# Kernel optimization log

Measured on AMD Instinct MI355X. Metric: run time of the kernel, lower is better.

The kernel has to match this reference:

```python
import jax, jax.numpy as jnp
import numpy as np

B, S, D, H, HD, L, V = 32, 512, 512, 8, 64, 6, 64000
EPS = 1e-5

def _layer_norm(x, g, b):
    mu = jnp.mean(x, axis=-1, keepdims=True)
    var = jnp.mean(jnp.square(x - mu), axis=-1, keepdims=True)
    return (x - mu) * jax.lax.rsqrt(var + EPS) * g + b

def _sinusoidal_pe():
    pos = np.arange(S)[:, None].astype(np.float32)
    div = np.exp(np.arange(0, D, 2).astype(np.float32) * -(np.log(10000.0) / D))
    pe = np.zeros((S, D), dtype=np.float32)
    pe[:, 0::2] = np.sin(pos * div)
    pe[:, 1::2] = np.cos(pos * div)
    return jnp.asarray(pe)

def setup_inputs() -> dict:
    key = jax.random.key(0)
    ks = jax.random.split(key, 8)
    std = 0.02
    return {
        'tokens': jax.random.randint(ks[0], (B, S), 0, V),
        'mask': jnp.ones((B, S), dtype=jnp.int32),
        'emb': jax.random.normal(ks[1], (V, D), jnp.float32) * std,
        'pe': _sinusoidal_pe(),
        'Wq': jax.random.normal(ks[2], (L, H, D, HD), jnp.float32) * std,
        'Wk': jax.random.normal(ks[3], (L, H, D, HD), jnp.float32) * std,
        'Wv': jax.random.normal(ks[4], (L, H, D, HD), jnp.float32) * std,
        'Wo': jax.random.normal(ks[5], (L, D, D), jnp.float32) * std,
        'ln1_g': jnp.ones((L, D), jnp.float32),
        'ln1_b': jnp.zeros((L, D), jnp.float32),
        'W1': jax.random.normal(ks[6], (L, D, 4 * D), jnp.float32) * std,
        'b1': jnp.zeros((L, 4 * D), jnp.float32),
        'W2': jax.random.normal(ks[7], (L, 4 * D, D), jnp.float32) * std,
        'b2': jnp.zeros((L, D), jnp.float32),
        'ln2_g': jnp.ones((L, D), jnp.float32),
        'ln2_b': jnp.zeros((L, D), jnp.float32),
    }

def reference(tokens, mask, emb, pe, Wq, Wk, Wv, Wo, ln1_g, ln1_b, W1, b1, W2, b2, ln2_g, ln2_b):
    # Eval mode: all dropouts are identity.
    x = emb[tokens] + pe[None, :S, :]               # [B,S,D]
    neg_inf = jnp.finfo(x.dtype).min
    mask_b = (mask == 0)[:, None, None, :]          # [B,1,1,S] broadcast over heads & queries
    scale = HD ** -0.5
    for l in range(L):
        q = jnp.einsum('bsd,hde->bhse', x, Wq[l])
        k = jnp.einsum('bsd,hde->bhse', x, Wk[l])
        v = jnp.einsum('bsd,hde->bhse', x, Wv[l])
        w = jnp.einsum('bhse,bhte->bhst', q, k) * scale
        w = jnp.where(mask_b, neg_inf, w)
        a = jax.nn.softmax(w, axis=-1)
        o = jnp.einsum('bhst,bhte->bhse', a, v)     # [B,H,S,HD]
        o = o.transpose(0, 2, 1, 3).reshape(x.shape[0], S, D)  # concat heads
        x = _layer_norm(x + o @ Wo[l], ln1_g[l], ln1_b[l])
        h = jax.nn.gelu(x @ W1[l] + b1[l], approximate=False) @ W2[l] + b2[l]
        x = _layer_norm(x + h, ln2_g[l], ln2_b[l])
    return x
```

## Files before the change

### kernel.cpp

```cpp
#include <hip/hip_runtime.h>

#define BB 32
#define SS 512
#define DD 512
#define HH 8
#define HDH 64
#define LL 6
#define DFF 2048
#define MM (BB*SS)

typedef __attribute__((ext_vector_type(4))) float f32x4;
typedef __attribute__((ext_vector_type(8))) short s16x8;
typedef __attribute__((ext_vector_type(4))) short s16x4;

__device__ __forceinline__ unsigned short f2bf(float f) {
    union { float f; unsigned u; } v; v.f = f;
    unsigned r = v.u + 0x7fffu + ((v.u >> 16) & 1u);
    return (unsigned short)(r >> 16);
}
__device__ __forceinline__ float bf2f(unsigned short b) {
    union { unsigned u; float f; } v; v.u = ((unsigned)b) << 16;
    return v.f;
}

__device__ __forceinline__ f32x4 mfma_bf16(s16x8 a, s16x8 b, f32x4 c) {
    asm("v_mfma_f32_16x16x32_bf16 %0, %1, %2, %0" : "+v"(c) : "v"(a), "v"(b));
    return c;
}

__device__ __forceinline__ void gload_lds16(const void* g, void* l) {
    __builtin_amdgcn_global_load_lds(
        (__attribute__((address_space(1))) void*)g,
        (__attribute__((address_space(3))) void*)l, 16, 0, 0);
}

__device__ __forceinline__ void tile_transpose_conv(
    const float* __restrict__ src, int srcPitch,
    unsigned short* __restrict__ dst, int dstPitch,
    float* lt)
{
    const int t = threadIdx.x;
    #pragma unroll
    for (int it = 0; it < 4; ++it) {
        int r = it * 16 + (t >> 4);
        int c = (t & 15) * 4;
        f32x4 v = *(const f32x4*)(src + (size_t)r * srcPitch + c);
        lt[r * 65 + c + 0] = v[0];
        lt[r * 65 + c + 1] = v[1];
        lt[r * 65 + c + 2] = v[2];
        lt[r * 65 + c + 3] = v[3];
    }
    __syncthreads();
    int nn = t >> 2;
    int kc = (t & 3) * 16;
    s16x8 o0, o1;
    #pragma unroll
    for (int i = 0; i < 8; ++i)  o0[i] = (short)f2bf(lt[(kc + i) * 65 + nn]);
    #pragma unroll
    for (int i = 0; i < 8; ++i)  o1[i] = (short)f2bf(lt[(kc + 8 + i) * 65 + nn]);
    *(s16x8*)(dst + (size_t)nn * dstPitch + kc) = o0;
    *(s16x8*)(dst + (size_t)nn * dstPitch + kc + 8) = o1;
}

__global__ __launch_bounds__(256) void k_tconv_qkv(const float* __restrict__ Wq,
                                                   const float* __restrict__ Wk,
                                                   const float* __restrict__ Wv,
                                                   unsigned short* __restrict__ dst) {
    __shared__ float lt[64 * 65];
    int bid = blockIdx.x;
    int which = bid / 384;
    int rem = bid - which * 384;
    int l = rem >> 6;
    int h = (rem >> 3) & 7;
    int kt = rem & 7;
    const float* W = which == 0 ? Wq : (which == 1 ? Wk : Wv);
    const float* srcT = W + (((size_t)(l * HH + h) * 512) + kt * 64) * 64;
    unsigned short* dstT = dst + ((size_t)l * 1536 + which * 512 + h * 64) * 512 + kt * 64;
    tile_transpose_conv(srcT, 64, dstT, 512, lt);
}

__global__ __launch_bounds__(256) void k_tconv_w(const float* __restrict__ src,
                                                 unsigned short* __restrict__ dst,
                                                 int K, int N) {
    __shared__ float lt[64 * 65];
    int tpb = (K >> 6) * (N >> 6);
    int bid = blockIdx.x;
    int l = bid / tpb;
    int rem = bid - l * tpb;
    int kt = rem / (N >> 6);
    int ntile = rem - kt * (N >> 6);
    const float* srcT = src + (size_t)l * K * N + (size_t)(kt * 64) * N + ntile * 64;
    unsigned short* dstT = dst + (size_t)l * N * K + (size_t)(ntile * 64) * K + kt * 64;
    tile_transpose_conv(srcT, N, dstT, K, lt);
}

__global__ __launch_bounds__(256) void k_embed(const int* __restrict__ tokens,
                                               const float* __restrict__ emb,
                                               const float* __restrict__ pe,
                                               float* __restrict__ x,
                                               unsigned short* __restrict__ xh) {
    int i = blockIdx.x * 256 + threadIdx.x;
    int row = i >> 7;
    int d4 = (i & 127) * 4;
    int srow = row & (SS - 1);
    int tok = tokens[row];
    f32x4 ev = *(const f32x4*)(emb + (size_t)tok*DD + d4);
    f32x4 pv = *(const f32x4*)(pe + (size_t)srow*DD + d4);
    f32x4 vv; s16x4 hv;
    #pragma unroll
    for (int j = 0; j < 4; ++j) {
        vv[j] = ev[j] + pv[j];
        hv[j] = (short)f2bf(vv[j]);
    }
    *(f32x4*)(x + (size_t)row*DD + d4) = vv;
    *(s16x4*)(xh + (size_t)row*DD + d4) = hv;
}

__global__ __launch_bounds__(128) void k_ln(const float* __restrict__ x,
                                            const unsigned short* __restrict__ y,
                                            const float* __restrict__ gg,
                                            const float* __restrict__ bb,
                                            float* __restrict__ xo,
                                            unsigned short* __restrict__ xh) {
    const int row = blockIdx.x;
    const int tid = threadIdx.x;
    __shared__ float red[4];
    f32x4 xv = *(const f32x4*)(x + (size_t)row*DD + tid*4);
    s16x4 yv = *(const s16x4*)(y + (size_t)row*DD + tid*4);
    f32x4 vv;
    #pragma unroll
    for (int j = 0; j < 4; ++j) vv[j] = xv[j] + bf2f((unsigned short)yv[j]);
    float sum = vv[0] + vv[1] + vv[2] + vv[3];
    #pragma unroll
    for (int off = 1; off < 64; off <<= 1) sum += __shfl_xor(sum, off);
    if ((tid & 63) == 0) red[tid >> 6] = sum;
    __syncthreads();
    float mu = (red[0] + red[1]) * (1.0f / 512.0f);
    float s2 = 0.0f;
    #pragma unroll
    for (int j = 0; j < 4; ++j) { float d = vv[j] - mu; s2 += d * d; }
    #pragma unroll
    for (int off = 1; off < 64; off <<= 1) s2 += __shfl_xor(s2, off);
    if ((tid & 63) == 0) red[2 + (tid >> 6)] = s2;
    __syncthreads();
    float var = (red[2] + red[3]) * (1.0f / 512.0f);
    float rs = rsqrtf(var + 1e-5f);
    f32x4 gv = *(const f32x4*)(gg + tid*4);
    f32x4 bv = *(const f32x4*)(bb + tid*4);
    f32x4 ov; s16x4 hv;
    #pragma unroll
    for (int j = 0; j < 4; ++j) {
        float o = (vv[j] - mu) * rs * gv[j] + bv[j];
        ov[j] = o;
        hv[j] = (short)f2bf(o);
    }
    *(f32x4*)(xo + (size_t)row*DD + tid*4) = ov;
    *(s16x4*)(xh + (size_t)row*DD + tid*4) = hv;
}

template<int EPI>
__global__ __launch_bounds__(256, 2) void k_gemm(
    const unsigned short* __restrict__ A, const unsigned short* __restrict__ Bt,
    unsigned short* __restrict__ ob,
    const float* __restrict__ bias, int N, int K, int nt)
{
    __shared__ short lds[2][2][4096];
    const int tid = threadIdx.x;
    const int lane = tid & 63;
    const int wid = tid >> 6;
    const int g = lane >> 4;
    const int t16 = lane & 15;

    int nwg = gridDim.x;
    int bid = blockIdx.x;
    int cpx = nwg >> 3;
    int swz = (bid & 7) * cpx + (bid >> 3);
    int bm = swz / nt;
    int bn = swz - bm * nt;

    const unsigned short* Ag = A  + (size_t)bm * 128 * K;
    const unsigned short* Bg = Bt + (size_t)bn * 128 * K;

    auto stage = [&](int buf, int k0) {
        #pragma unroll
        for (int i = 0; i < 2; ++i) {
            int slot = i * 256 + tid;
            int r = slot >> 2;
            int j = slot & 3;
            int js = j ^ ((r >> 1) & 3);
            size_t go = (size_t)r * K + k0 + js * 8;
            int lo = i * 2048 + wid * 512;
            gload_lds16(Ag + go, &lds[buf][0][lo]);
            gload_lds16(Bg + go, &lds[buf][1][lo]);
        }
    };

    f32x4 acc[4][4];
    #pragma unroll
    for (int a_ = 0; a_ < 4; ++a_)
        #pragma unroll
        for (int b_ = 0; b_ < 4; ++b_) acc[a_][b_] = (f32x4){0.f, 0.f, 0.f, 0.f};

    const int wm = wid >> 1, wn = wid & 1;
    stage(0, 0);
    __syncthreads();
    int nk = K >> 5;
    int buf = 0;
    for (int kt = 0; kt < nk; ++kt) {
        if (kt + 1 < nk) stage(buf ^ 1, (kt + 1) << 5);
        s16x8 af[4], bf_[4];
        #pragma unroll
        for (int mt = 0; mt < 4; ++mt) {
            int r = wm * 64 + mt * 16 + t16;
            af[mt] = *(const s16x8*)&lds[buf][0][r * 32 + ((g ^ ((r >> 1) & 3)) << 3)];
        }
        #pragma unroll
        for (int nt_ = 0; nt_ < 4; ++nt_) {
            int r = wn * 64 + nt_ * 16 + t16;
            bf_[nt_] = *(const s16x8*)&lds[buf][1][r * 32 + ((g ^ ((r >> 1) & 3)) << 3)];
        }
        #pragma unroll
        for (int mt = 0; mt < 4; ++mt)
            #pragma unroll
            for (int nt_ = 0; nt_ < 4; ++nt_)
                acc[mt][nt_] = mfma_bf16(af[mt], bf_[nt_], acc[mt][nt_]);
        __syncthreads();
        buf ^= 1;
    }

    #pragma unroll
    for (int mt = 0; mt < 4; ++mt)
        #pragma unroll
        for (int nt_ = 0; nt_ < 4; ++nt_) {
            int row0 = bm * 128 + wm * 64 + mt * 16 + g * 4;
            int col  = bn * 128 + wn * 64 + nt_ * 16 + t16;
            f32x4 v = acc[mt][nt_];
            float bv = (EPI == 2) ? bias[col] : 0.0f;
            #pragma unroll
            for (int r_ = 0; r_ < 4; ++r_) {
                size_t idx = (size_t)(row0 + r_) * N + col;
                if (EPI == 0) {
                    ob[idx] = f2bf(v[r_]);
                } else {
                    float tv = v[r_] + bv;
                    float ge = 0.5f * tv * (1.0f + erff(tv * 0.70710678118f));
                    ob[idx] = f2bf(ge);
                }
            }
        }
}

__global__ __launch_bounds__(512, 2) void k_gemm8(
    const unsigned short* __restrict__ A, const unsigned short* __restrict__ Bt,
    unsigned short* __restrict__ ob,
    const float* __restrict__ bias, int N, int K, int nt)
{
    extern __shared__ short lds[];
    const int tid = threadIdx.x;
    const int lane = tid & 63;
    const int wid = tid >> 6;
    const int g = lane >> 4;
    const int t16 = lane & 15;
    const int wm = wid >> 2, wn = wid & 3;

    int nwg = gridDim.x;
    int bid = blockIdx.x;
    int cpx = nwg >> 3;
    int swz = (bid & 7) * cpx + (bid >> 3);
    int bm = swz / nt;
    int bn = swz - bm * nt;

    const unsigned short* Ag = A  + (size_t)bm * 256 * K;
    const unsigned short* Bg = Bt + (size_t)bn * 128 * K;

    auto stage_unit = [&](int slot, int t, int unit) {
        const int k0 = t << 6;
        const unsigned short* src = (unit == 2) ? Bg : (Ag + (unit ? (size_t)128 * K : 0));
        short* dst0 = lds + slot * 24576 + (unit == 2 ? 16384 : unit * 8192);
        #pragma unroll
        for (int rr = 0; rr < 2; ++rr) {
            int rb = rr * 64 + wid * 8;
            int r_in = rb + (lane >> 3);
            int c = (lane & 7) ^ (r_in & 7);
            gload_lds16(src + (size_t)r_in * K + k0 + c * 8, dst0 + rb * 64);
        }
    };

    f32x4 acc[8][2];
    #pragma unroll
    for (int a_ = 0; a_ < 8; ++a_)
        #pragma unroll
        for (int b_ = 0; b_ < 2; ++b_) acc[a_][b_] = (f32x4){0.f, 0.f, 0.f, 0.f};

    const int nk = K >> 6;
    stage_unit(0, 0, 0); stage_unit(0, 0, 1); stage_unit(0, 0, 2);
    stage_unit(1, 1, 0); stage_unit(1, 1, 1); stage_unit(1, 1, 2);

    int slot = 0;
    for (int t = 0; t < nk; ++t) {
        if (t + 1 < nk) asm volatile("s_waitcnt vmcnt(6)" ::: "memory");
        else            asm volatile("s_waitcnt vmcnt(0)" ::: "memory");
        __builtin_amdgcn_s_barrier();
        __builtin_amdgcn_sched_barrier(0);

        int s2 = slot + 2; if (s2 >= 3) s2 -= 3;
        const short* As = lds + slot * 24576;
        const short* Bs = As + 16384;

        if (t + 2 < nk) { stage_unit(s2, t + 2, 0); stage_unit(s2, t + 2, 1); }
        s16x8 bfr[2][2];
        #pragma unroll
        for (int nn = 0; nn < 2; ++nn) {
            int row = wn * 32 + nn * 16 + t16;
            #pragma unroll
            for (int kk = 0; kk < 2; ++kk)
                bfr[nn][kk] = *(const s16x8*)&Bs[row * 64 + (((kk * 4 + g) ^ (row & 7)) << 3)];
        }
        {
            s16x8 afr[4][2];
            #pragma unroll
            for (int mm = 0; mm < 4; ++mm) {
                int row = wm * 128 + mm * 16 + t16;
                #pragma unroll
                for (int kk = 0; kk < 2; ++kk)
                    afr[mm][kk] = *(const s16x8*)&As[row * 64 + (((kk * 4 + g) ^ (row & 7)) << 3)];
            }
            __builtin_amdgcn_sched_barrier(0);
            __builtin_amdgcn_s_setprio(1);
            #pragma unroll
            for (int mm = 0; mm < 4; ++mm)
                #pragma unroll
                for (int nn = 0; nn < 2; ++nn)
                    #pragma unroll
                    for (int kk = 0; kk < 2; ++kk)
                        acc[mm][nn] = mfma_bf16(afr[mm][kk], bfr[nn][kk], acc[mm][nn]);
            __builtin_amdgcn_s_setprio(0);
            __builtin_amdgcn_sched_barrier(0);
        }
        if (t + 2 < nk) stage_unit(s2, t + 2, 2);
        {
            s16x8 afr[4][2];
            #pragma unroll
            for (int mm = 0; mm < 4; ++mm) {
                int row = wm * 128 + (mm + 4) * 16 + t16;
                #pragma unroll
                for (int kk = 0; kk < 2; ++kk)
                    afr[mm][kk] = *(const s16x8*)&As[row * 64 + (((kk * 4 + g) ^ (row & 7)) << 3)];
            }
            __builtin_amdgcn_sched_barrier(0);
            __builtin_amdgcn_s_setprio(1);
            #pragma unroll
            for (int mm = 0; mm < 4; ++mm)
                #pragma unroll
                for (int nn = 0; nn < 2; ++nn)
                    #pragma unroll
                    for (int kk = 0; kk < 2; ++kk)
                        acc[mm + 4][nn] = mfma_bf16(afr[mm][kk], bfr[nn][kk], acc[mm + 4][nn]);
            __builtin_amdgcn_s_setprio(0);
            __builtin_amdgcn_sched_barrier(0);
        }
        slot = slot + 1 == 3 ? 0 : slot + 1;
    }

    #pragma unroll
    for (int mm = 0; mm < 8; ++mm)
        #pragma unroll
        for (int nn = 0; nn < 2; ++nn) {
            int row0 = bm * 256 + wm * 128 + mm * 16 + g * 4;
            int col  = bn * 128 + wn * 32 + nn * 16 + t16;
            f32x4 v = acc[mm][nn];
            float bv = bias[col];
            #pragma unroll
            for (int r_ = 0; r_ < 4; ++r_)
                ob[(size_t)(row0 + r_) * N + col] = f2bf(v[r_] + bv);
        }
}

__global__ __launch_bounds__(1024, 4) void k_attn(
    const unsigned short* __restrict__ qkv, const int* __restrict__ mask,
    unsigned short* __restrict__ o)
{
    extern __shared__ short smem[];
    short* Kl = smem;
    short* Vl = smem + 32768;
    const int tid = threadIdx.x;
    const int lane = tid & 63, wid = tid >> 6;
    short* Pl = smem + 65536 + wid * 1024;
    const int b = blockIdx.x >> 3, h = blockIdx.x & 7;
    const unsigned short* base = qkv + (size_t)b * SS * 1536;
    const int qc = h * 64, kc = 512 + h * 64, vc = 1024 + h * 64;

    for (int c = tid; c < 4096; c += 1024) {
        int t = c >> 3, j = c & 7;
        s16x8 kv = *(const s16x8*)(base + (size_t)t * 1536 + kc + j * 8);
        *(s16x8*)(Kl + t * 64 + ((j ^ (t & 7)) << 3)) = kv;
    }
    {
        int unit = tid >> 1, half = tid & 1;
        int t0 = (unit >> 3) << 3, e0 = (unit & 7) << 3;
        s16x8 r0 = *(const s16x8*)(base + (size_t)(t0 + half*4 + 0) * 1536 + vc + e0);
        s16x8 r1 = *(const s16x8*)(base + (size_t)(t0 + half*4 + 1) * 1536 + vc + e0);
        s16x8 r2 = *(const s16x8*)(base + (size_t)(t0 + half*4 + 2) * 1536 + vc + e0);
        s16x8 r3 = *(const s16x8*)(base + (size_t)(t0 + half*4 + 3) * 1536 + vc + e0);
        #pragma unroll
        for (int j = 0; j < 8; ++j) {
            int e = e0 + j;
            int slot = (t0 >> 3) ^ (e & 7) ^ ((e >> 3) & 7);
            s16x4 w = (s16x4){r0[j], r1[j], r2[j], r3[j]};
            *(s16x4*)(Vl + e * 512 + (slot << 3) + (half << 2)) = w;
        }
    }
    const int g = lane >> 4, t16 = lane & 15;
    unsigned mbits = 0;
    for (int n2 = 0; n2 < 32; ++n2)
        if (mask[b * SS + n2 * 16 + t16] != 0) mbits |= (1u << n2);
    __syncthreads();

    for (int qi = 0; qi < 2; ++qi) {
        const int q0 = (wid * 2 + qi) * 16;
        s16x8 aq[2];
        #pragma unroll
        for (int ks = 0; ks < 2; ++ks)
            aq[ks] = *(const s16x8*)(base + (size_t)(q0 + t16) * 1536 + qc + ks * 32 + g * 8);

        f32x4 oacc[4];
        #pragma unroll
        for (int eo = 0; eo < 4; ++eo) oacc[eo] = (f32x4){0.f, 0.f, 0.f, 0.f};
        float mx[4] = {-3.0e38f, -3.0e38f, -3.0e38f, -3.0e38f};
        float ls[4] = {0.f, 0.f, 0.f, 0.f};

        for (int tc = 0; tc < 4; ++tc) {
            f32x4 s[8];
            #pragma unroll
            for (int n2 = 0; n2 < 8; ++n2) s[n2] = (f32x4){0.f, 0.f, 0.f, 0.f};
            #pragma unroll
            for (int n2 = 0; n2 < 8; ++n2) {
                int t = tc * 128 + n2 * 16 + t16;
                #pragma unroll
                for (int ks = 0; ks < 2; ++ks) {
                    int blk = ks * 4 + g;
                    s16x8 bk = *(const s16x8*)(Kl + t * 64 + ((blk ^ (t & 7)) << 3));
                    s[n2] = mfma_bf16(aq[ks], bk, s[n2]);
                }
            }
            #pragma unroll
            for (int n2 = 0; n2 < 8; ++n2) {
                bool val = (mbits >> (tc * 8 + n2)) & 1u;
                #pragma unroll
                for (int r_ = 0; r_ < 4; ++r_)
                    s[n2][r_] = val ? s[n2][r_] * 0.125f : -3.0e38f;
            }
            float sc[4];
            #pragma unroll
            for (int r_ = 0; r_ < 4; ++r_) {
                float m = s[0][r_];
                #pragma unroll
                for (int n2 = 1; n2 < 8; ++n2) m = fmaxf(m, s[n2][r_]);
                #pragma unroll
                for (int off = 1; off < 16; off <<= 1) m = fmaxf(m, __shfl_xor(m, off));
                float mn = fmaxf(mx[r_], m);
                sc[r_] = __expf(mx[r_] - mn);
                mx[r_] = mn;
                ls[r_] *= sc[r_];
            }
            #pragma unroll
            for (int eo = 0; eo < 4; ++eo)
                #pragma unroll
                for (int r_ = 0; r_ < 4; ++r_) oacc[eo][r_] *= sc[r_];
            #pragma unroll
            for (int n2 = 0; n2 < 8; ++n2)
                #pragma unroll
                for (int r_ = 0; r_ < 4; ++r_)
                    s[n2][r_] = __expf(s[n2][r_] - mx[r_]);
            #pragma unroll
            for (int r_ = 0; r_ < 4; ++r_) {
                float t = 0.f;
                #pragma unroll
                for (int n2 = 0; n2 < 8; ++n2) t += s[n2][r_];
                #pragma unroll
                for (int off = 1; off < 16; off <<= 1) t += __shfl_xor(t, off);
                ls[r_] += t;
            }
            #pragma unroll
            for (int c4 = 0; c4 < 2; ++c4) {
                #pragma unroll
                for (int k4 = 0; k4 < 4; ++k4) {
                    int n2 = c4 * 4 + k4;
                    #pragma unroll
                    for (int r_ = 0; r_ < 4; ++r_) {
                        int qq = g * 4 + r_;
                        int kk = k4 * 16 + t16;
                        Pl[qq * 64 + (((kk >> 3) ^ (qq & 7)) << 3) + (kk & 7)] =
                            (short)f2bf(s[n2][r_]);
                    }
                }
                #pragma unroll
                for (int ks2 = 0; ks2 < 2; ++ks2) {
                    int kk = ks2 * 32 + g * 8;
                    s16x8 pa = *(const s16x8*)(Pl + t16 * 64 + (((kk >> 3) ^ (t16 & 7)) << 3));
                    int tg = tc * 128 + c4 * 64 + kk;
                    #pragma unroll
                    for (int eo = 0; eo < 4; ++eo) {
                        int e = eo * 16 + t16;
                        int slot = (tg >> 3) ^ (e & 7) ^ ((e >> 3) & 7);
                        s16x8 bv = *(const s16x8*)(Vl + e * 512 + (slot << 3));
                        oacc[eo] = mfma_bf16(pa, bv, oacc[eo]);
                    }
                }
            }
        }
        #pragma unroll
        for (int eo = 0; eo < 4; ++eo)
            #pragma unroll
            for (int r_ = 0; r_ < 4; ++r_) {
                int row = q0 + g * 4 + r_;
                int e = eo * 16 + t16;
                o[((size_t)b * SS + row) * DD + h * HDH + e] =
                    f2bf(oacc[eo][r_] / ls[r_]);
            }
    }
}

extern "C" void kernel_launch(void* const* d_in, const int* in_sizes, int n_in,
                              void* d_out, int out_size, void* d_ws, size_t ws_size,
                              hipStream_t stream)
{
    const int*   tokens = (const int*)d_in[0];
    const int*   mask   = (const int*)d_in[1];
    const float* emb    = (const float*)d_in[2];
    const float* pe     = (const float*)d_in[3];
    const float* Wq     = (const float*)d_in[4];
    const float* Wk     = (const float*)d_in[5];
    const float* Wv     = (const float*)d_in[6];
    const float* Wo     = (const float*)d_in[7];
    const float* l1g    = (const float*)d_in[8];
    const float* l1b    = (const float*)d_in[9];
    const float* W1     = (const float*)d_in[10];
    const float* b1     = (const float*)d_in[11];
    const float* W2     = (const float*)d_in[12];
    const float* b2     = (const float*)d_in[13];
    const float* l2g    = (const float*)d_in[14];
    const float* l2b    = (const float*)d_in[15];

    char* p = (char*)d_ws;
    auto alloc = [&](size_t bytes) { char* r = p; p += (bytes + 255) & ~(size_t)255; return r; };
    unsigned short* wqkv_t = (unsigned short*)alloc((size_t)LL*3*DD*DD*2);
    unsigned short* wo_t   = (unsigned short*)alloc((size_t)LL*DD*DD*2);
    unsigned short* w1_t   = (unsigned short*)alloc((size_t)LL*DD*DFF*2);
    unsigned short* w2_t   = (unsigned short*)alloc((size_t)LL*DD*DFF*2);
    float*          x      = (float*)alloc((size_t)MM*DD*4);
    unsigned short* xh     = (unsigned short*)alloc((size_t)MM*DD*2);
    unsigned short* qkvb   = (unsigned short*)alloc((size_t)MM*1536*2);
    unsigned short* obuf   = (unsigned short*)alloc((size_t)MM*DD*2);
    unsigned short* ybufb  = (unsigned short*)alloc((size_t)MM*DD*2);
    unsigned short* hbuf   = qkvb;

    k_tconv_qkv<<<1152, 256, 0, stream>>>(Wq, Wk, Wv, wqkv_t);
    k_tconv_w<<<384, 256, 0, stream>>>(Wo, wo_t, 512, 512);
    k_tconv_w<<<1536, 256, 0, stream>>>(W1, w1_t, 512, 2048);
    k_tconv_w<<<1536, 256, 0, stream>>>(W2, w2_t, 2048, 512);
    k_embed<<<8192, 256, 0, stream>>>(tokens, emb, pe, x, xh);

    hipFuncSetAttribute((const void*)k_attn,
                        hipFuncAttributeMaxDynamicSharedMemorySize, 163840);
    hipFuncSetAttribute((const void*)k_gemm8,
                        hipFuncAttributeMaxDynamicSharedMemorySize, 147456);

    for (int l = 0; l < LL; ++l) {
        const unsigned short* wqkvl = wqkv_t + (size_t)l*3*DD*DD;
        const unsigned short* wol   = wo_t   + (size_t)l*DD*DD;
        const unsigned short* w1l   = w1_t   + (size_t)l*DD*DFF;
        const unsigned short* w2l   = w2_t   + (size_t)l*DD*DFF;

        k_gemm<0><<<1536, 256, 0, stream>>>(xh, wqkvl, qkvb, nullptr, 1536, 512, 12);
        k_attn<<<256, 1024, 163840, stream>>>(qkvb, mask, obuf);
        k_gemm<0><<<512, 256, 0, stream>>>(obuf, wol, ybufb, nullptr, 512, 512, 4);
        k_ln<<<16384, 128, 0, stream>>>(x, ybufb, l1g + l*DD, l1b + l*DD, x, xh);
        k_gemm<2><<<2048, 256, 0, stream>>>(xh, w1l, hbuf, b1 + (size_t)l*DFF, 2048, 512, 16);
        k_gemm8<<<256, 512, 147456, stream>>>(hbuf, w2l, ybufb, b2 + (size_t)l*DD, 512, 2048, 4);
        float* xout = (l == LL - 1) ? (float*)d_out : x;
        k_ln<<<16384, 128, 0, stream>>>(x, ybufb, l2g + l*DD, l2b + l*DD, xout, xh);
    }
}
```

Measured before the change: 1.383 ms.

## Pipeline K/V chunks through double-buffered LDS in attention and fold scale into Wk

The attention kernel now streams K and V in 128-token chunks through double-buffered LDS, using async global-to-LDS loads for K and register-staged transposed writes for V. The next chunk's loads overlap with compute on the current one, and LDS use drops from 160KB to 96KB. Both query tiles per wave are processed together within each chunk. The softmax scale and log2(e) are folded into the bf16 Wk conversion so the kernel can use raw v_exp_f32 (exp2) with no per-score multiply. The change adds a barrier per chunk, and exp2 on prescaled bf16 keys shifts numerics slightly.

```diff
diff --git a/kernel.cpp b/kernel.cpp
--- a/kernel.cpp
+++ b/kernel.cpp
@@ -22,6 +22,9 @@
     union { unsigned u; float f; } v; v.u = ((unsigned)b) << 16;
     return v.f;
 }
+__device__ __forceinline__ float exp2_fast(float x) {
+    float r; asm("v_exp_f32 %0, %1" : "=v"(r) : "v"(x)); return r;
+}
 
 __device__ __forceinline__ f32x4 mfma_bf16(s16x8 a, s16x8 b, f32x4 c) {
     asm("v_mfma_f32_16x16x32_bf16 %0, %1, %2, %0" : "+v"(c) : "v"(a), "v"(b));
@@ -37,7 +40,7 @@
 __device__ __forceinline__ void tile_transpose_conv(
     const float* __restrict__ src, int srcPitch,
     unsigned short* __restrict__ dst, int dstPitch,
-    float* lt)
+    float* lt, float scale)
 {
     const int t = threadIdx.x;
     #pragma unroll
@@ -55,9 +58,9 @@
     int kc = (t & 3) * 16;
     s16x8 o0, o1;
     #pragma unroll
-    for (int i = 0; i < 8; ++i)  o0[i] = (short)f2bf(lt[(kc + i) * 65 + nn]);
-    #pragma unroll
-    for (int i = 0; i < 8; ++i)  o1[i] = (short)f2bf(lt[(kc + 8 + i) * 65 + nn]);
+    for (int i = 0; i < 8; ++i)  o0[i] = (short)f2bf(lt[(kc + i) * 65 + nn] * scale);
+    #pragma unroll
+    for (int i = 0; i < 8; ++i)  o1[i] = (short)f2bf(lt[(kc + 8 + i) * 65 + nn] * scale);
     *(s16x8*)(dst + (size_t)nn * dstPitch + kc) = o0;
     *(s16x8*)(dst + (size_t)nn * dstPitch + kc + 8) = o1;
 }
@@ -74,9 +77,10 @@
     int h = (rem >> 3) & 7;
     int kt = rem & 7;
     const float* W = which == 0 ? Wq : (which == 1 ? Wk : Wv);
+    float scale = (which == 1) ? 0.1803368801111601f : 1.0f;
     const float* srcT = W + (((size_t)(l * HH + h) * 512) + kt * 64) * 64;
     unsigned short* dstT = dst + ((size_t)l * 1536 + which * 512 + h * 64) * 512 + kt * 64;
-    tile_transpose_conv(srcT, 64, dstT, 512, lt);
+    tile_transpose_conv(srcT, 64, dstT, 512, lt, scale);
 }
 
 __global__ __launch_bounds__(256) void k_tconv_w(const float* __restrict__ src,
@@ -91,7 +95,7 @@
     int ntile = rem - kt * (N >> 6);
     const float* srcT = src + (size_t)l * K * N + (size_t)(kt * 64) * N + ntile * 64;
     unsigned short* dstT = dst + (size_t)l * N * K + (size_t)(ntile * 64) * K + kt * 64;
-    tile_transpose_conv(srcT, N, dstT, K, lt);
+    tile_transpose_conv(srcT, N, dstT, K, lt, 1.0f);
 }
 
 __global__ __launch_bounds__(256) void k_embed(const int* __restrict__ tokens,
@@ -376,79 +380,104 @@
         }
 }
 
-__global__ __launch_bounds__(1024, 4) void k_attn(
+__global__ __launch_bounds__(1024, 1) void k_attn(
     const unsigned short* __restrict__ qkv, const int* __restrict__ mask,
     unsigned short* __restrict__ o)
 {
     extern __shared__ short smem[];
-    short* Kl = smem;
-    short* Vl = smem + 32768;
     const int tid = threadIdx.x;
     const int lane = tid & 63, wid = tid >> 6;
-    short* Pl = smem + 65536 + wid * 1024;
+    const int g = lane >> 4, t16 = lane & 15;
     const int b = blockIdx.x >> 3, h = blockIdx.x & 7;
     const unsigned short* base = qkv + (size_t)b * SS * 1536;
     const int qc = h * 64, kc = 512 + h * 64, vc = 1024 + h * 64;
-
-    for (int c = tid; c < 4096; c += 1024) {
-        int t = c >> 3, j = c & 7;
-        s16x8 kv = *(const s16x8*)(base + (size_t)t * 1536 + kc + j * 8);
-        *(s16x8*)(Kl + t * 64 + ((j ^ (t & 7)) << 3)) = kv;
-    }
-    {
-        int unit = tid >> 1, half = tid & 1;
-        int t0 = (unit >> 3) << 3, e0 = (unit & 7) << 3;
-        s16x8 r0 = *(const s16x8*)(base + (size_t)(t0 + half*4 + 0) * 1536 + vc + e0);
-        s16x8 r1 = *(const s16x8*)(base + (size_t)(t0 + half*4 + 1) * 1536 + vc + e0);
-        s16x8 r2 = *(const s16x8*)(base + (size_t)(t0 + half*4 + 2) * 1536 + vc + e0);
-        s16x8 r3 = *(const s16x8*)(base + (size_t)(t0 + half*4 + 3) * 1536 + vc + e0);
-        #pragma unroll
-        for (int j = 0; j < 8; ++j) {
-            int e = e0 + j;
-            int slot = (t0 >> 3) ^ (e & 7) ^ ((e >> 3) & 7);
-            s16x4 w = (s16x4){r0[j], r1[j], r2[j], r3[j]};
-            *(s16x4*)(Vl + e * 512 + (slot << 3) + (half << 2)) = w;
-        }
-    }
-    const int g = lane >> 4, t16 = lane & 15;
+    short* Pl = smem + 32768 + wid * 1024;
+
+    auto stageK = [&](int buf, int c) {
+        int row = tid >> 3;
+        int js = (tid & 7) ^ (row & 7);
+        gload_lds16(base + (size_t)(c * 128 + row) * 1536 + kc + js * 8,
+                    smem + buf * 8192 + wid * 512);
+    };
+    const int kp = (tid & 511) >> 3;
+    const int e0 = (tid & 7) * 8;
+    const int k0 = kp * 2;
+    auto readV = [&](int c, s16x8& va, s16x8& vb) {
+        va = *(const s16x8*)(base + (size_t)(c * 128 + k0) * 1536 + vc + e0);
+        vb = *(const s16x8*)(base + (size_t)(c * 128 + k0 + 1) * 1536 + vc + e0);
+    };
+    auto writeV = [&](int buf, s16x8 va, s16x8 vb) {
+        short* V = smem + 16384 + buf * 8192;
+        #pragma unroll
+        for (int i = 0; i < 8; ++i) {
+            int e = e0 + i;
+            int slot = (k0 >> 3) ^ (e & 7) ^ ((e >> 3) & 7);
+            unsigned pk = (unsigned)(unsigned short)va[i] |
+                          ((unsigned)(unsigned short)vb[i] << 16);
+            *(unsigned*)&V[e * 128 + slot * 8 + (k0 & 7)] = pk;
+        }
+    };
+
+    s16x8 aq[2][2];
+    #pragma unroll
+    for (int qi = 0; qi < 2; ++qi) {
+        int q0 = (wid * 2 + qi) * 16;
+        #pragma unroll
+        for (int ks = 0; ks < 2; ++ks)
+            aq[qi][ks] = *(const s16x8*)(base + (size_t)(q0 + t16) * 1536 + qc + ks * 32 + g * 8);
+    }
     unsigned mbits = 0;
     for (int n2 = 0; n2 < 32; ++n2)
         if (mask[b * SS + n2 * 16 + t16] != 0) mbits |= (1u << n2);
+
+    stageK(0, 0);
+    {
+        s16x8 va, vb;
+        if (tid < 512) { readV(0, va, vb); writeV(0, va, vb); }
+    }
     __syncthreads();
 
-    for (int qi = 0; qi < 2; ++qi) {
-        const int q0 = (wid * 2 + qi) * 16;
-        s16x8 aq[2];
-        #pragma unroll
-        for (int ks = 0; ks < 2; ++ks)
-            aq[ks] = *(const s16x8*)(base + (size_t)(q0 + t16) * 1536 + qc + ks * 32 + g * 8);
-
-        f32x4 oacc[4];
-        #pragma unroll
-        for (int eo = 0; eo < 4; ++eo) oacc[eo] = (f32x4){0.f, 0.f, 0.f, 0.f};
-        float mx[4] = {-3.0e38f, -3.0e38f, -3.0e38f, -3.0e38f};
-        float ls[4] = {0.f, 0.f, 0.f, 0.f};
-
-        for (int tc = 0; tc < 4; ++tc) {
+    f32x4 oacc[2][4];
+    float mx[2][4], ls[2][4];
+    #pragma unroll
+    for (int qi = 0; qi < 2; ++qi)
+        #pragma unroll
+        for (int i = 0; i < 4; ++i) {
+            oacc[qi][i] = (f32x4){0.f, 0.f, 0.f, 0.f};
+            mx[qi][i] = -3.0e38f; ls[qi][i] = 0.f;
+        }
+
+    #pragma unroll
+    for (int c = 0; c < 4; ++c) {
+        const int cur = c & 1;
+        const short* Kc = smem + cur * 8192;
+        const short* Vc = smem + 16384 + cur * 8192;
+        s16x8 nva, nvb;
+        if (c < 3) {
+            stageK(cur ^ 1, c + 1);
+            if (tid < 512) readV(c + 1, nva, nvb);
+        }
+        #pragma unroll
+        for (int qi = 0; qi < 2; ++qi) {
             f32x4 s[8];
             #pragma unroll
             for (int n2 = 0; n2 < 8; ++n2) s[n2] = (f32x4){0.f, 0.f, 0.f, 0.f};
             #pragma unroll
             for (int n2 = 0; n2 < 8; ++n2) {
-                int t = tc * 128 + n2 * 16 + t16;
+                int t = n2 * 16 + t16;
                 #pragma unroll
                 for (int ks = 0; ks < 2; ++ks) {
                     int blk = ks * 4 + g;
-                    s16x8 bk = *(const s16x8*)(Kl + t * 64 + ((blk ^ (t & 7)) << 3));
-                    s[n2] = mfma_bf16(aq[ks], bk, s[n2]);
+                    s16x8 bk = *(const s16x8*)&Kc[t * 64 + ((blk ^ (t & 7)) << 3)];
+                    s[n2] = mfma_bf16(aq[qi][ks], bk, s[n2]);
                 }
             }
             #pragma unroll
             for (int n2 = 0; n2 < 8; ++n2) {
-                bool val = (mbits >> (tc * 8 + n2)) & 1u;
+                bool val = (mbits >> (c * 8 + n2)) & 1u;
                 #pragma unroll
                 for (int r_ = 0; r_ < 4; ++r_)
-                    s[n2][r_] = val ? s[n2][r_] * 0.125f : -3.0e38f;
+                    s[n2][r_] = val ? s[n2][r_] : -3.0e38f;
             }
             float sc[4];
             #pragma unroll
@@ -458,20 +487,20 @@
                 for (int n2 = 1; n2 < 8; ++n2) m = fmaxf(m, s[n2][r_]);
                 #pragma unroll
                 for (int off = 1; off < 16; off <<= 1) m = fmaxf(m, __shfl_xor(m, off));
-                float mn = fmaxf(mx[r_], m);
-                sc[r_] = __expf(mx[r_] - mn);
-                mx[r_] = mn;
-                ls[r_] *= sc[r_];
+                float mn = fmaxf(mx[qi][r_], m);
+                sc[r_] = exp2_fast(mx[qi][r_] - mn);
+                mx[qi][r_] = mn;
+                ls[qi][r_] *= sc[r_];
             }
             #pragma unroll
             for (int eo = 0; eo < 4; ++eo)
                 #pragma unroll
-                for (int r_ = 0; r_ < 4; ++r_) oacc[eo][r_] *= sc[r_];
+                for (int r_ = 0; r_ < 4; ++r_) oacc[qi][eo][r_] *= sc[r_];
             #pragma unroll
             for (int n2 = 0; n2 < 8; ++n2)
                 #pragma unroll
                 for (int r_ = 0; r_ < 4; ++r_)
-                    s[n2][r_] = __expf(s[n2][r_] - mx[r_]);
+                    s[n2][r_] = exp2_fast(s[n2][r_] - mx[qi][r_]);
             #pragma unroll
             for (int r_ = 0; r_ < 4; ++r_) {
                 float t = 0.f;
@@ -479,7 +508,7 @@
                 for (int n2 = 0; n2 < 8; ++n2) t += s[n2][r_];
                 #pragma unroll
                 for (int off = 1; off < 16; off <<= 1) t += __shfl_xor(t, off);
-                ls[r_] += t;
+                ls[qi][r_] += t;
             }
             #pragma unroll
             for (int c4 = 0; c4 < 2; ++c4) {
@@ -498,17 +527,24 @@
                 for (int ks2 = 0; ks2 < 2; ++ks2) {
                     int kk = ks2 * 32 + g * 8;
                     s16x8 pa = *(const s16x8*)(Pl + t16 * 64 + (((kk >> 3) ^ (t16 & 7)) << 3));
-                    int tg = tc * 128 + c4 * 64 + kk;
+                    int tg2 = c4 * 64 + kk;
                     #pragma unroll
                     for (int eo = 0; eo < 4; ++eo) {
                         int e = eo * 16 + t16;
-                        int slot = (tg >> 3) ^ (e & 7) ^ ((e >> 3) & 7);
-                        s16x8 bv = *(const s16x8*)(Vl + e * 512 + (slot << 3));
-                        oacc[eo] = mfma_bf16(pa, bv, oacc[eo]);
+                        int slot = (tg2 >> 3) ^ (e & 7) ^ ((e >> 3) & 7);
+                        s16x8 bv = *(const s16x8*)&Vc[e * 128 + (slot << 3)];
+                        oacc[qi][eo] = mfma_bf16(pa, bv, oacc[qi][eo]);
                     }
                 }
             }
         }
+        if (c < 3 && tid < 512) writeV(cur ^ 1, nva, nvb);
+        __syncthreads();
+    }
+
+    #pragma unroll
+    for (int qi = 0; qi < 2; ++qi) {
+        int q0 = (wid * 2 + qi) * 16;
         #pragma unroll
         for (int eo = 0; eo < 4; ++eo)
             #pragma unroll
@@ -516,7 +552,7 @@
                 int row = q0 + g * 4 + r_;
                 int e = eo * 16 + t16;
                 o[((size_t)b * SS + row) * DD + h * HDH + e] =
-                    f2bf(oacc[eo][r_] / ls[r_]);
+                    f2bf(oacc[qi][eo][r_] / ls[qi][r_]);
             }
     }
 }
@@ -562,7 +598,7 @@
     k_embed<<<8192, 256, 0, stream>>>(tokens, emb, pe, x, xh);
 
     hipFuncSetAttribute((const void*)k_attn,
-                        hipFuncAttributeMaxDynamicSharedMemorySize, 163840);
+                        hipFuncAttributeMaxDynamicSharedMemorySize, 98304);
     hipFuncSetAttribute((const void*)k_gemm8,
                         hipFuncAttributeMaxDynamicSharedMemorySize, 147456);
 
@@ -573,7 +609,7 @@
         const unsigned short* w2l   = w2_t   + (size_t)l*DD*DFF;
 
         k_gemm<0><<<1536, 256, 0, stream>>>(xh, wqkvl, qkvb, nullptr, 1536, 512, 12);
-        k_attn<<<256, 1024, 163840, stream>>>(qkvb, mask, obuf);
+        k_attn<<<256, 1024, 98304, stream>>>(qkvb, mask, obuf);
         k_gemm<0><<<512, 256, 0, stream>>>(obuf, wol, ybufb, nullptr, 512, 512, 4);
         k_ln<<<16384, 128, 0, stream>>>(x, ybufb, l1g + l*DD, l1b + l*DD, x, xh);
         k_gemm<2><<<2048, 256, 0, stream>>>(xh, w1l, hbuf, b1 + (size_t)l*DFF, 2048, 512, 16);
```

After: 1.899 ms. 1.37x slower.

## Fold softmax scale and log2e into Wk; use exp2 and direct-to-LDS K loads

Applied to the files above, without the earlier changes.

Pre-multiplies the K weights by scale*log2(e) during the one-time weight conversion. This removes the per-score multiply in attention and lets the softmax use the raw v_exp_f32 (exp2) instruction instead of __expf. It also replaces the register-staged K tile load into LDS with global_load_lds direct transfers that keep the same XOR swizzle. The trade-off is that K is rounded to bf16 after scaling, and the LDS layout now depends on the lane ordering of the direct loads.

```diff
diff --git a/kernel.cpp b/kernel.cpp
--- a/kernel.cpp
+++ b/kernel.cpp
@@ -22,6 +22,9 @@
     union { unsigned u; float f; } v; v.u = ((unsigned)b) << 16;
     return v.f;
 }
+__device__ __forceinline__ float exp2_fast(float x) {
+    float r; asm("v_exp_f32 %0, %1" : "=v"(r) : "v"(x)); return r;
+}
 
 __device__ __forceinline__ f32x4 mfma_bf16(s16x8 a, s16x8 b, f32x4 c) {
     asm("v_mfma_f32_16x16x32_bf16 %0, %1, %2, %0" : "+v"(c) : "v"(a), "v"(b));
@@ -37,7 +40,7 @@
 __device__ __forceinline__ void tile_transpose_conv(
     const float* __restrict__ src, int srcPitch,
     unsigned short* __restrict__ dst, int dstPitch,
-    float* lt)
+    float* lt, float scale)
 {
     const int t = threadIdx.x;
     #pragma unroll
@@ -55,9 +58,9 @@
     int kc = (t & 3) * 16;
     s16x8 o0, o1;
     #pragma unroll
-    for (int i = 0; i < 8; ++i)  o0[i] = (short)f2bf(lt[(kc + i) * 65 + nn]);
-    #pragma unroll
-    for (int i = 0; i < 8; ++i)  o1[i] = (short)f2bf(lt[(kc + 8 + i) * 65 + nn]);
+    for (int i = 0; i < 8; ++i)  o0[i] = (short)f2bf(lt[(kc + i) * 65 + nn] * scale);
+    #pragma unroll
+    for (int i = 0; i < 8; ++i)  o1[i] = (short)f2bf(lt[(kc + 8 + i) * 65 + nn] * scale);
     *(s16x8*)(dst + (size_t)nn * dstPitch + kc) = o0;
     *(s16x8*)(dst + (size_t)nn * dstPitch + kc + 8) = o1;
 }
@@ -74,9 +77,10 @@
     int h = (rem >> 3) & 7;
     int kt = rem & 7;
     const float* W = which == 0 ? Wq : (which == 1 ? Wk : Wv);
+    float scale = (which == 1) ? 0.18033688011116048f : 1.0f;
     const float* srcT = W + (((size_t)(l * HH + h) * 512) + kt * 64) * 64;
     unsigned short* dstT = dst + ((size_t)l * 1536 + which * 512 + h * 64) * 512 + kt * 64;
-    tile_transpose_conv(srcT, 64, dstT, 512, lt);
+    tile_transpose_conv(srcT, 64, dstT, 512, lt, scale);
 }
 
 __global__ __launch_bounds__(256) void k_tconv_w(const float* __restrict__ src,
@@ -91,7 +95,7 @@
     int ntile = rem - kt * (N >> 6);
     const float* srcT = src + (size_t)l * K * N + (size_t)(kt * 64) * N + ntile * 64;
     unsigned short* dstT = dst + (size_t)l * N * K + (size_t)(ntile * 64) * K + kt * 64;
-    tile_transpose_conv(srcT, N, dstT, K, lt);
+    tile_transpose_conv(srcT, N, dstT, K, lt, 1.0f);
 }
 
 __global__ __launch_bounds__(256) void k_embed(const int* __restrict__ tokens,
@@ -390,10 +394,16 @@
     const unsigned short* base = qkv + (size_t)b * SS * 1536;
     const int qc = h * 64, kc = 512 + h * 64, vc = 1024 + h * 64;
 
-    for (int c = tid; c < 4096; c += 1024) {
-        int t = c >> 3, j = c & 7;
-        s16x8 kv = *(const s16x8*)(base + (size_t)t * 1536 + kc + j * 8);
-        *(s16x8*)(Kl + t * 64 + ((j ^ (t & 7)) << 3)) = kv;
+    {
+        int row0 = (tid >> 3);
+        int s = tid & 7;
+        #pragma unroll
+        for (int it = 0; it < 4; ++it) {
+            int row = it * 128 + row0;
+            int j = s ^ (row & 7);
+            gload_lds16(base + (size_t)row * 1536 + kc + j * 8,
+                        Kl + it * 8192 + wid * 512);
+        }
     }
     {
         int unit = tid >> 1, half = tid & 1;
@@ -448,7 +458,7 @@
                 bool val = (mbits >> (tc * 8 + n2)) & 1u;
                 #pragma unroll
                 for (int r_ = 0; r_ < 4; ++r_)
-                    s[n2][r_] = val ? s[n2][r_] * 0.125f : -3.0e38f;
+                    s[n2][r_] = val ? s[n2][r_] : -3.0e38f;
             }
             float sc[4];
             #pragma unroll
@@ -459,7 +469,7 @@
                 #pragma unroll
                 for (int off = 1; off < 16; off <<= 1) m = fmaxf(m, __shfl_xor(m, off));
                 float mn = fmaxf(mx[r_], m);
-                sc[r_] = __expf(mx[r_] - mn);
+                sc[r_] = exp2_fast(mx[r_] - mn);
                 mx[r_] = mn;
                 ls[r_] *= sc[r_];
             }
@@ -471,7 +481,7 @@
             for (int n2 = 0; n2 < 8; ++n2)
                 #pragma unroll
                 for (int r_ = 0; r_ < 4; ++r_)
-                    s[n2][r_] = __expf(s[n2][r_] - mx[r_]);
+                    s[n2][r_] = exp2_fast(s[n2][r_] - mx[r_]);
             #pragma unroll
             for (int r_ = 0; r_ < 4; ++r_) {
                 float t = 0.f;
```

New measurement: 1.371 ms. Within noise of the previous version (-0.8%).
